# Optimization experiments

Measured on AMD Instinct MI355X. Metric: run time of the kernel, lower is better.

Reference implementation:

```python
import jax, jax.numpy as jnp
from jax import lax
import numpy as np

T, B, I, H, O = 512, 64, 512, 1024, 512


def setup_inputs() -> dict:
    key = jax.random.key(0)
    ks = jax.random.split(key, 8)
    s_ih = 1.0 / np.sqrt(I)
    s_hh = 1.0 / np.sqrt(H)
    return {
        "x": jax.random.normal(ks[0], (T, B, I), dtype=jnp.float32),
        "hidden": jnp.zeros((1, B, H), dtype=jnp.float32),
        "W_ih": jax.random.normal(ks[1], (H, I), dtype=jnp.float32) * s_ih,
        "W_hh": jax.random.normal(ks[2], (H, H), dtype=jnp.float32) * s_hh,
        "b_ih": jax.random.normal(ks[3], (H,), dtype=jnp.float32) * s_hh,
        "b_hh": jax.random.normal(ks[4], (H,), dtype=jnp.float32) * s_hh,
        "W_fc": jax.random.normal(ks[5], (O, H), dtype=jnp.float32) * s_hh,
        "b_fc": jax.random.normal(ks[6], (O,), dtype=jnp.float32) * s_hh,
    }


def reference(x, hidden, W_ih, W_hh, b_ih, b_hh, W_fc, b_fc):
    # Precompute the input projection for all timesteps as one big GEMM.
    # xp: [T, B, H]
    xp = jnp.einsum("tbi,hi->tbh", x, W_ih) + b_ih

    h0 = hidden[0]  # [B, H]

    def step(h, xt):
        # PyTorch RNN (tanh): h_t = tanh(W_ih x_t + b_ih + W_hh h_{t-1} + b_hh)
        h_new = jnp.tanh(xt + h @ W_hh.T + b_hh)
        return h_new, h_new

    h_last, hs = lax.scan(step, h0, xp)  # hs: [T, B, H]

    # fc applied to flattened [T*B, H] hidden states
    out = hs.reshape(-1, hs.shape[-1]) @ W_fc.T + b_fc  # [T*B, O]
    return out, h_last[None]  # ([T*B, O], [1, B, H])
```

## Files before the change

kernel.cpp:

```cpp
#include <hip/hip_runtime.h>

typedef __attribute__((ext_vector_type(8))) short bf16x8;
typedef __attribute__((ext_vector_type(4))) float f32x4;

#define T_N 512
#define I_N 512
#define H_N 1024
#define O_N 512
#define NMEM 16
#define NTHR 512
#define COLS_H 64
#define COLS_FC 32
#define KW 192
#define KWFC 128
#define AP_STRIDE 1544
#define RST 21

__device__ __forceinline__ unsigned short f2bf(float f) {
  unsigned int u = __float_as_uint(f);
  u += 0x7fffu + ((u >> 16) & 1u);
  return (unsigned short)(u >> 16);
}
__device__ __forceinline__ bf16x8 cvt8f(const float* __restrict__ p) {
  float4 a = *(const float4*)p;
  float4 b = *(const float4*)(p + 4);
  bf16x8 r;
  r[0] = (short)f2bf(a.x); r[1] = (short)f2bf(a.y);
  r[2] = (short)f2bf(a.z); r[3] = (short)f2bf(a.w);
  r[4] = (short)f2bf(b.x); r[5] = (short)f2bf(b.y);
  r[6] = (short)f2bf(b.z); r[7] = (short)f2bf(b.w);
  return r;
}

__device__ __forceinline__ void coh_store_b32(unsigned int* p, unsigned int v) {
  asm volatile("global_store_dword %0, %1, off sc0 sc1" :: "v"(p), "v"(v) : "memory");
}
__device__ __forceinline__ unsigned int coh_load_b32(const unsigned int* p) {
  unsigned int r;
  asm volatile("global_load_dword %0, %1, off sc0 sc1\n\t"
               "s_waitcnt vmcnt(0)" : "=v"(r) : "v"(p) : "memory");
  return r;
}

__global__ __launch_bounds__(NTHR, 2) void rnn_fused(
    const float* __restrict__ x, const float* __restrict__ hidden,
    const float* __restrict__ Wih, const float* __restrict__ Whh,
    const float* __restrict__ bih, const float* __restrict__ bhh,
    const float* __restrict__ Wfc, const float* __restrict__ bfc,
    float* __restrict__ out, float* __restrict__ hlast,
    unsigned short* __restrict__ hx, unsigned int* __restrict__ flags)
{
  __shared__ __align__(16) unsigned short Apan[16 * AP_STRIDE];
  __shared__ __align__(16) float R [8 * COLS_H  * RST];
  __shared__ __align__(16) float R2[8 * COLS_FC * RST];

  const int tid = threadIdx.x;
  const int l = tid & 63, w = tid >> 6;
  const int bid = blockIdx.x;
  const int c = bid & 3;
  const int m = bid >> 2;
  const int b0 = c * 16;
  const int cbh = m * COLS_H;
  const int cbfc = m * COLS_FC;
  unsigned short* hxc = hx + (size_t)c * 2 * 16 * H_N;
  unsigned int* flg = flags + c * 64;

  bf16x8 Bh[6][4];
  {
    const int kb0 = w * KW + ((l >> 4) << 3);
#pragma unroll
    for (int kst = 0; kst < 6; ++kst) {
      const int k = kb0 + kst * 32;
#pragma unroll
      for (int f = 0; f < 4; ++f) {
        const int col = cbh + f * 16 + (l & 15);
        const float* src = (k < H_N) ? (Whh + (size_t)col * H_N + k)
                                     : (Wih + (size_t)col * I_N + (k - H_N));
        Bh[kst][f] = cvt8f(src);
      }
    }
  }
  bf16x8 Bf[4][2];
  {
    const int kb0 = w * KWFC + ((l >> 4) << 3);
#pragma unroll
    for (int kst = 0; kst < 4; ++kst)
#pragma unroll
      for (int f = 0; f < 2; ++f) {
        const int col = cbfc + f * 16 + (l & 15);
        Bf[kst][f] = cvt8f(Wfc + (size_t)col * H_N + kb0 + kst * 32);
      }
  }

  const int hrow = (w << 1) + (l >> 5);
  const int hcp  = l & 31;
  const float pb0 = bih[cbh + 2 * hcp]     + bhh[cbh + 2 * hcp];
  const float pb1 = bih[cbh + 2 * hcp + 1] + bhh[cbh + 2 * hcp + 1];
  const int frow = hrow;
  const int fcol = l & 31;
  const float bfv = bfc[cbfc + fcol];

  const int q0 = tid, q1 = 512 + tid;

#pragma unroll
  for (int i = 0; i < 4; ++i) {
    const int q = i * 512 + tid;
    const int row = q >> 7, hc8 = (q & 127) << 3;
    bf16x8 v = cvt8f(hidden + (size_t)(b0 + row) * H_N + hc8);
    *(bf16x8*)(Apan + row * AP_STRIDE + hc8) = v;
  }
  *(bf16x8*)(Apan + (q0 >> 6) * AP_STRIDE + H_N + ((q0 & 63) << 3)) =
      cvt8f(x + (size_t)(b0 + (q0 >> 6)) * I_N + ((q0 & 63) << 3));
  *(bf16x8*)(Apan + (q1 >> 6) * AP_STRIDE + H_N + ((q1 & 63) << 3)) =
      cvt8f(x + (size_t)(b0 + (q1 >> 6)) * I_N + ((q1 & 63) << 3));
  bf16x8 xr0 = cvt8f(x + (size_t)(64 + b0 + (q0 >> 6)) * I_N + ((q0 & 63) << 3));
  bf16x8 xr1 = cvt8f(x + (size_t)(64 + b0 + (q1 >> 6)) * I_N + ((q1 & 63) << 3));
  __syncthreads();

  for (int t = 0; t < T_N; ++t) {
    {
      f32x4 acc[4] = {};
      const int abase = (l & 15) * AP_STRIDE + w * KW + ((l >> 4) << 3);
#pragma unroll
      for (int kst = 0; kst < 6; ++kst) {
        bf16x8 a = *(const bf16x8*)(Apan + abase + kst * 32);
#pragma unroll
        for (int f = 0; f < 4; ++f)
          acc[f] = __builtin_amdgcn_mfma_f32_16x16x32_bf16(a, Bh[kst][f], acc[f], 0, 0, 0);
      }
#pragma unroll
      for (int f = 0; f < 4; ++f)
        *(f32x4*)(R + (size_t)(w * COLS_H + f * 16 + (l & 15)) * RST + ((l >> 4) << 2)) = acc[f];
    }
    if (t > 0) {
      f32x4 afc[2] = {};
      const int ab2 = (l & 15) * AP_STRIDE + w * KWFC + ((l >> 4) << 3);
#pragma unroll
      for (int kst = 0; kst < 4; ++kst) {
        bf16x8 a = *(const bf16x8*)(Apan + ab2 + kst * 32);
        afc[0] = __builtin_amdgcn_mfma_f32_16x16x32_bf16(a, Bf[kst][0], afc[0], 0, 0, 0);
        afc[1] = __builtin_amdgcn_mfma_f32_16x16x32_bf16(a, Bf[kst][1], afc[1], 0, 0, 0);
      }
#pragma unroll
      for (int f = 0; f < 2; ++f)
        *(f32x4*)(R2 + (size_t)(w * COLS_FC + f * 16 + (l & 15)) * RST + ((l >> 4) << 2)) = afc[f];
    }
    __syncthreads();

    {
      float v0 = pb0, v1 = pb1;
#pragma unroll
      for (int kk = 0; kk < 8; ++kk) {
        v0 += R[(size_t)(kk * COLS_H + 2 * hcp)     * RST + hrow];
        v1 += R[(size_t)(kk * COLS_H + 2 * hcp + 1) * RST + hrow];
      }
      const float h0 = tanhf(v0), h1 = tanhf(v1);
      const unsigned int packed =
          (unsigned int)f2bf(h0) | ((unsigned int)f2bf(h1) << 16);
      unsigned int* dst = (unsigned int*)(hxc + (size_t)((t & 1) * 16 + hrow) * H_N + cbh + 2 * hcp);
      coh_store_b32(dst, packed);
      if (t == T_N - 1) {
        float2 fv; fv.x = h0; fv.y = h1;
        *(float2*)(hlast + (size_t)(b0 + hrow) * H_N + cbh + 2 * hcp) = fv;
      }
    }
    asm volatile("s_waitcnt vmcnt(0)" ::: "memory");
    __syncthreads();
    if (tid == 0) coh_store_b32(&flg[m], (unsigned int)(t + 1));

    if (t > 0) {
      float v = bfv;
#pragma unroll
      for (int kk = 0; kk < 8; ++kk)
        v += R2[(size_t)(kk * COLS_FC + fcol) * RST + frow];
      out[(size_t)((t - 1) * 64 + b0 + frow) * O_N + cbfc + fcol] = v;
    }
    if (t + 1 < T_N) {
      *(bf16x8*)(Apan + (q0 >> 6) * AP_STRIDE + H_N + ((q0 & 63) << 3)) = xr0;
      *(bf16x8*)(Apan + (q1 >> 6) * AP_STRIDE + H_N + ((q1 & 63) << 3)) = xr1;
      if (t + 2 < T_N) {
        xr0 = cvt8f(x + (size_t)((t + 2) * 64 + b0 + (q0 >> 6)) * I_N + ((q0 & 63) << 3));
        xr1 = cvt8f(x + (size_t)((t + 2) * 64 + b0 + (q1 >> 6)) * I_N + ((q1 & 63) << 3));
      }
    }

    if (tid < NMEM) {
      while (coh_load_b32(&flg[tid]) < (unsigned int)(t + 1))
        __builtin_amdgcn_s_sleep(1);
    }
    __syncthreads();

    {
      const unsigned long long* src =
          (const unsigned long long*)(hxc + (size_t)(t & 1) * 16 * H_N);
      unsigned long long hv[8];
#pragma unroll
      for (int i = 0; i < 8; ++i)
        asm volatile("global_load_dwordx2 %0, %1, off sc0 sc1"
                     : "=v"(hv[i]) : "v"(src + tid + 512 * i) : "memory");
      asm volatile("s_waitcnt vmcnt(0)" ::: "memory");
      __builtin_amdgcn_sched_barrier(0);
#pragma unroll
      for (int i = 0; i < 8; ++i) {
        const int c8 = tid + 512 * i;
        const int row = c8 >> 8, col = (c8 & 255) << 2;
        *(unsigned long long*)(Apan + row * AP_STRIDE + col) = hv[i];
      }
    }
    __syncthreads();
  }

  {
    f32x4 afc[2] = {};
    const int ab2 = (l & 15) * AP_STRIDE + w * KWFC + ((l >> 4) << 3);
#pragma unroll
    for (int kst = 0; kst < 4; ++kst) {
      bf16x8 a = *(const bf16x8*)(Apan + ab2 + kst * 32);
      afc[0] = __builtin_amdgcn_mfma_f32_16x16x32_bf16(a, Bf[kst][0], afc[0], 0, 0, 0);
      afc[1] = __builtin_amdgcn_mfma_f32_16x16x32_bf16(a, Bf[kst][1], afc[1], 0, 0, 0);
    }
#pragma unroll
    for (int f = 0; f < 2; ++f)
      *(f32x4*)(R2 + (size_t)(w * COLS_FC + f * 16 + (l & 15)) * RST + ((l >> 4) << 2)) = afc[f];
    __syncthreads();
    float v = bfv;
#pragma unroll
    for (int kk = 0; kk < 8; ++kk)
      v += R2[(size_t)(kk * COLS_FC + fcol) * RST + frow];
    out[(size_t)(511 * 64 + b0 + frow) * O_N + cbfc + fcol] = v;
  }
}

extern "C" void kernel_launch(void* const* d_in, const int* in_sizes, int n_in,
                              void* d_out, int out_size, void* d_ws, size_t ws_size,
                              hipStream_t stream) {
  const float* x   = (const float*)d_in[0];
  const float* hid = (const float*)d_in[1];
  const float* Wih = (const float*)d_in[2];
  const float* Whh = (const float*)d_in[3];
  const float* bih = (const float*)d_in[4];
  const float* bhh = (const float*)d_in[5];
  const float* Wfc = (const float*)d_in[6];
  const float* bfc = (const float*)d_in[7];

  float* out   = (float*)d_out;
  float* hlast = out + (size_t)32768 * 512;

  unsigned int*   flags = (unsigned int*)d_ws;
  unsigned short* hx    = (unsigned short*)((char*)d_ws + 1024);

  hipMemsetAsync(flags, 0, 1024, stream);
  rnn_fused<<<64, NTHR, 0, stream>>>(x, hid, Wih, Whh, bih, bhh, Wfc, bfc,
                                     out, hlast, hx, flags);
}
```

Baseline: 1.795 ms.

## Split batch across 8 clusters and replace flag barrier with canary-polled data slots

Doubles the grid to 128 blocks, with each cluster now handling 8 batch rows instead of 16; the MFMA A panel is zero-padded to 16 rows. The per-step flag barrier is replaced by fp32 hidden-state slots in a 4-deep ring. Consumers poll the data itself until no canary values remain, and producers re-poison the slot two steps ahead, which removes a full store-wait, syncthreads and flag round trip per step. Wave specialisation assigns the tanh work to waves 0-3 and the x prefetch to waves 4-7; the costs are wasted MFMA work on padding rows, fp32 traffic instead of bf16, and bounded spin caps that could silently proceed on a timeout.

Result: no change. 1.801 ms (+0.4%).

```diff
diff --git a/kernel.cpp b/kernel.cpp
--- a/kernel.cpp
+++ b/kernel.cpp
@@ -2,19 +2,26 @@
 
 typedef __attribute__((ext_vector_type(8))) short bf16x8;
 typedef __attribute__((ext_vector_type(4))) float f32x4;
+typedef __attribute__((ext_vector_type(2))) float f32x2;
 
 #define T_N 512
 #define I_N 512
 #define H_N 1024
 #define O_N 512
+#define NCL 8
 #define NMEM 16
+#define BATCH 8
 #define NTHR 512
 #define COLS_H 64
 #define COLS_FC 32
 #define KW 192
 #define KWFC 128
 #define AP_STRIDE 1544
-#define RST 21
+#define AP_ROWS 20
+#define RST 9
+#define CANARY 0xFFFFFFFFu
+#define HS_CAP  20000000
+#define POLL_CAP 200000
 
 __device__ __forceinline__ unsigned short f2bf(float f) {
   unsigned int u = __float_as_uint(f);
@@ -31,15 +38,35 @@
   r[6] = (short)f2bf(b.z); r[7] = (short)f2bf(b.w);
   return r;
 }
-
-__device__ __forceinline__ void coh_store_b32(unsigned int* p, unsigned int v) {
+__device__ __forceinline__ bf16x8 cvt8v(float4 a, float4 b) {
+  bf16x8 r;
+  r[0] = (short)f2bf(a.x); r[1] = (short)f2bf(a.y);
+  r[2] = (short)f2bf(a.z); r[3] = (short)f2bf(a.w);
+  r[4] = (short)f2bf(b.x); r[5] = (short)f2bf(b.y);
+  r[6] = (short)f2bf(b.z); r[7] = (short)f2bf(b.w);
+  return r;
+}
+
+__device__ __forceinline__ void st_sc01(unsigned int* p, unsigned int v) {
   asm volatile("global_store_dword %0, %1, off sc0 sc1" :: "v"(p), "v"(v) : "memory");
 }
-__device__ __forceinline__ unsigned int coh_load_b32(const unsigned int* p) {
+__device__ __forceinline__ void st2_sc01(float* p, f32x2 v) {
+  asm volatile("global_store_dwordx2 %0, %1, off sc0 sc1" :: "v"(p), "v"(v) : "memory");
+}
+__device__ __forceinline__ void st2u_sc01(float* p, unsigned long long v) {
+  asm volatile("global_store_dwordx2 %0, %1, off sc0 sc1" :: "v"(p), "v"(v) : "memory");
+}
+__device__ __forceinline__ unsigned int ld_sc01(const unsigned int* p) {
   unsigned int r;
-  asm volatile("global_load_dword %0, %1, off sc0 sc1\n\t"
-               "s_waitcnt vmcnt(0)" : "=v"(r) : "v"(p) : "memory");
+  asm volatile("global_load_dword %0, %1, off sc0 sc1\n\ts_waitcnt vmcnt(0)"
+               : "=v"(r) : "v"(p) : "memory");
   return r;
+}
+__device__ __forceinline__ void ld4_sc01(uint4* d, const void* p) {
+  asm volatile("global_load_dwordx4 %0, %1, off sc0 sc1" : "=v"(*d) : "v"(p) : "memory");
+}
+__device__ __forceinline__ void ld4_rawf(float4* d, const void* p) {
+  asm volatile("global_load_dwordx4 %0, %1, off" : "=v"(*d) : "v"(p) : "memory");
 }
 
 __global__ __launch_bounds__(NTHR, 2) void rnn_fused(
@@ -48,26 +75,25 @@
     const float* __restrict__ bih, const float* __restrict__ bhh,
     const float* __restrict__ Wfc, const float* __restrict__ bfc,
     float* __restrict__ out, float* __restrict__ hlast,
-    unsigned short* __restrict__ hx, unsigned int* __restrict__ flags)
+    float* __restrict__ hslot, unsigned int* __restrict__ flags)
 {
-  __shared__ __align__(16) unsigned short Apan[16 * AP_STRIDE];
+  __shared__ __align__(16) unsigned short Apan[AP_ROWS * AP_STRIDE];
   __shared__ __align__(16) float R [8 * COLS_H  * RST];
   __shared__ __align__(16) float R2[8 * COLS_FC * RST];
 
   const int tid = threadIdx.x;
-  const int l = tid & 63, w = tid >> 6;
+  const int l = tid & 63, wv = tid >> 6;
   const int bid = blockIdx.x;
-  const int c = bid & 3;
-  const int m = bid >> 2;
-  const int b0 = c * 16;
+  const int c = bid & 7;
+  const int m = bid >> 3;
+  const int b0 = c * BATCH;
   const int cbh = m * COLS_H;
   const int cbfc = m * COLS_FC;
-  unsigned short* hxc = hx + (size_t)c * 2 * 16 * H_N;
-  unsigned int* flg = flags + c * 64;
+  float* slotc = hslot + (size_t)c * 4 * BATCH * H_N;
 
   bf16x8 Bh[6][4];
   {
-    const int kb0 = w * KW + ((l >> 4) << 3);
+    const int kb0 = wv * KW + ((l >> 4) << 3);
 #pragma unroll
     for (int kst = 0; kst < 6; ++kst) {
       const int k = kb0 + kst * 32;
@@ -82,45 +108,64 @@
   }
   bf16x8 Bf[4][2];
   {
-    const int kb0 = w * KWFC + ((l >> 4) << 3);
+    const int kb0 = wv * KWFC + ((l >> 4) << 3);
 #pragma unroll
     for (int kst = 0; kst < 4; ++kst)
 #pragma unroll
-      for (int f = 0; f < 2; ++f) {
-        const int col = cbfc + f * 16 + (l & 15);
-        Bf[kst][f] = cvt8f(Wfc + (size_t)col * H_N + kb0 + kst * 32);
-      }
-  }
-
-  const int hrow = (w << 1) + (l >> 5);
-  const int hcp  = l & 31;
-  const float pb0 = bih[cbh + 2 * hcp]     + bhh[cbh + 2 * hcp];
-  const float pb1 = bih[cbh + 2 * hcp + 1] + bhh[cbh + 2 * hcp + 1];
-  const int frow = hrow;
-  const int fcol = l & 31;
-  const float bfv = bfc[cbfc + fcol];
-
-  const int q0 = tid, q1 = 512 + tid;
-
-#pragma unroll
-  for (int i = 0; i < 4; ++i) {
-    const int q = i * 512 + tid;
-    const int row = q >> 7, hc8 = (q & 127) << 3;
-    bf16x8 v = cvt8f(hidden + (size_t)(b0 + row) * H_N + hc8);
-    *(bf16x8*)(Apan + row * AP_STRIDE + hc8) = v;
-  }
-  *(bf16x8*)(Apan + (q0 >> 6) * AP_STRIDE + H_N + ((q0 & 63) << 3)) =
-      cvt8f(x + (size_t)(b0 + (q0 >> 6)) * I_N + ((q0 & 63) << 3));
-  *(bf16x8*)(Apan + (q1 >> 6) * AP_STRIDE + H_N + ((q1 & 63) << 3)) =
-      cvt8f(x + (size_t)(b0 + (q1 >> 6)) * I_N + ((q1 & 63) << 3));
-  bf16x8 xr0 = cvt8f(x + (size_t)(64 + b0 + (q0 >> 6)) * I_N + ((q0 & 63) << 3));
-  bf16x8 xr1 = cvt8f(x + (size_t)(64 + b0 + (q1 >> 6)) * I_N + ((q1 & 63) << 3));
+      for (int f = 0; f < 2; ++f)
+        Bf[kst][f] = cvt8f(Wfc + (size_t)(cbfc + f * 16 + (l & 15)) * H_N + kb0 + kst * 32);
+  }
+
+  const int rrow = (tid >> 5) & 7;
+  const int rcp  = tid & 31;
+  const float pb0 = bih[cbh + 2 * rcp]     + bhh[cbh + 2 * rcp];
+  const float pb1 = bih[cbh + 2 * rcp + 1] + bhh[cbh + 2 * rcp + 1];
+  const float bfv = bfc[cbfc + rcp];
+
+  for (int q = tid; q < (8 * AP_STRIDE) / 4; q += NTHR)
+    ((unsigned long long*)(Apan + 8 * AP_STRIDE))[q] = 0ULL;
+  {
+    int q = tid;
+#pragma unroll
+    for (int i = 0; i < 2; ++i, q += NTHR) {
+      const int row = q >> 7, col8 = (q & 127) << 3;
+      *(bf16x8*)(Apan + row * AP_STRIDE + col8) =
+          cvt8f(hidden + (size_t)(b0 + row) * H_N + col8);
+    }
+  }
+  {
+    const int row = tid >> 6, col8 = (tid & 63) << 3;
+    *(bf16x8*)(Apan + row * AP_STRIDE + H_N + col8) =
+        cvt8f(x + (size_t)(b0 + row) * I_N + col8);
+  }
+  float4 xf0, xf1, xf2, xf3;
+  if (wv >= 4) {
+    const int u = tid & 255;
+    const float* p0 = x + ((size_t)64 + b0 + (u >> 6)) * I_N + ((u & 63) << 3);
+    ld4_rawf(&xf0, p0); ld4_rawf(&xf1, p0 + 4);
+    ld4_rawf(&xf2, p0 + 4 * I_N); ld4_rawf(&xf3, p0 + 4 * I_N + 4);
+  }
+
+  if (tid < 256) {
+#pragma unroll
+    for (int s = 0; s < 4; ++s)
+      st2u_sc01(slotc + (size_t)(s * BATCH + rrow) * H_N + cbh + 2 * rcp,
+                0xFFFFFFFFFFFFFFFFull);
+  }
+  asm volatile("s_waitcnt vmcnt(0)" ::: "memory");
+  __syncthreads();
+  if (tid == 0) st_sc01(&flags[c * 64 + m], 1u);
+  if (tid < NMEM) {
+    int it = 0;
+    while (ld_sc01(&flags[c * 64 + tid]) < 1u && ++it < HS_CAP)
+      if (it > 64) __builtin_amdgcn_s_sleep(1);
+  }
   __syncthreads();
 
   for (int t = 0; t < T_N; ++t) {
     {
       f32x4 acc[4] = {};
-      const int abase = (l & 15) * AP_STRIDE + w * KW + ((l >> 4) << 3);
+      const int abase = (l & 15) * AP_STRIDE + wv * KW + ((l >> 4) << 3);
 #pragma unroll
       for (int kst = 0; kst < 6; ++kst) {
         bf16x8 a = *(const bf16x8*)(Apan + abase + kst * 32);
@@ -128,106 +173,113 @@
         for (int f = 0; f < 4; ++f)
           acc[f] = __builtin_amdgcn_mfma_f32_16x16x32_bf16(a, Bh[kst][f], acc[f], 0, 0, 0);
       }
-#pragma unroll
-      for (int f = 0; f < 4; ++f)
-        *(f32x4*)(R + (size_t)(w * COLS_H + f * 16 + (l & 15)) * RST + ((l >> 4) << 2)) = acc[f];
+      if (l < 32) {
+#pragma unroll
+        for (int f = 0; f < 4; ++f)
+          *(f32x4*)(R + (size_t)(wv * COLS_H + f * 16 + (l & 15)) * RST + ((l >> 4) << 2)) = acc[f];
+      }
     }
     if (t > 0) {
       f32x4 afc[2] = {};
-      const int ab2 = (l & 15) * AP_STRIDE + w * KWFC + ((l >> 4) << 3);
+      const int ab2 = (l & 15) * AP_STRIDE + wv * KWFC + ((l >> 4) << 3);
 #pragma unroll
       for (int kst = 0; kst < 4; ++kst) {
         bf16x8 a = *(const bf16x8*)(Apan + ab2 + kst * 32);
         afc[0] = __builtin_amdgcn_mfma_f32_16x16x32_bf16(a, Bf[kst][0], afc[0], 0, 0, 0);
         afc[1] = __builtin_amdgcn_mfma_f32_16x16x32_bf16(a, Bf[kst][1], afc[1], 0, 0, 0);
       }
-#pragma unroll
-      for (int f = 0; f < 2; ++f)
-        *(f32x4*)(R2 + (size_t)(w * COLS_FC + f * 16 + (l & 15)) * RST + ((l >> 4) << 2)) = afc[f];
+      if (l < 32) {
+        *(f32x4*)(R2 + (size_t)(wv * COLS_FC + (l & 15)) * RST + ((l >> 4) << 2)) = afc[0];
+        *(f32x4*)(R2 + (size_t)(wv * COLS_FC + 16 + (l & 15)) * RST + ((l >> 4) << 2)) = afc[1];
+      }
     }
     __syncthreads();
 
-    {
+    if (wv < 4) {
       float v0 = pb0, v1 = pb1;
 #pragma unroll
       for (int kk = 0; kk < 8; ++kk) {
-        v0 += R[(size_t)(kk * COLS_H + 2 * hcp)     * RST + hrow];
-        v1 += R[(size_t)(kk * COLS_H + 2 * hcp + 1) * RST + hrow];
+        v0 += R[(size_t)(kk * COLS_H + 2 * rcp)     * RST + rrow];
+        v1 += R[(size_t)(kk * COLS_H + 2 * rcp + 1) * RST + rrow];
       }
       const float h0 = tanhf(v0), h1 = tanhf(v1);
-      const unsigned int packed =
-          (unsigned int)f2bf(h0) | ((unsigned int)f2bf(h1) << 16);
-      unsigned int* dst = (unsigned int*)(hxc + (size_t)((t & 1) * 16 + hrow) * H_N + cbh + 2 * hcp);
-      coh_store_b32(dst, packed);
+      f32x2 hv; hv[0] = h0; hv[1] = h1;
+      st2_sc01(slotc + (size_t)((t & 3) * BATCH + rrow) * H_N + cbh + 2 * rcp, hv);
+      st2u_sc01(slotc + (size_t)(((t + 2) & 3) * BATCH + rrow) * H_N + cbh + 2 * rcp,
+                0xFFFFFFFFFFFFFFFFull);
       if (t == T_N - 1) {
         float2 fv; fv.x = h0; fv.y = h1;
-        *(float2*)(hlast + (size_t)(b0 + hrow) * H_N + cbh + 2 * hcp) = fv;
-      }
-    }
-    asm volatile("s_waitcnt vmcnt(0)" ::: "memory");
+        *(float2*)(hlast + (size_t)(b0 + rrow) * H_N + cbh + 2 * rcp) = fv;
+      }
+    } else {
+      if (t + 1 < T_N) {
+        asm volatile("s_waitcnt vmcnt(0)" ::: "memory");
+        const int u = tid & 255;
+        *(bf16x8*)(Apan + (u >> 6) * AP_STRIDE + H_N + ((u & 63) << 3)) = cvt8v(xf0, xf1);
+        *(bf16x8*)(Apan + ((u >> 6) + 4) * AP_STRIDE + H_N + ((u & 63) << 3)) = cvt8v(xf2, xf3);
+        if (t + 2 < T_N) {
+          const float* p0 = x + ((size_t)(t + 2) * 64 + b0 + (u >> 6)) * I_N + ((u & 63) << 3);
+          ld4_rawf(&xf0, p0); ld4_rawf(&xf1, p0 + 4);
+          ld4_rawf(&xf2, p0 + 4 * I_N); ld4_rawf(&xf3, p0 + 4 * I_N + 4);
+        }
+      }
+    }
+
+    if (t > 0 && tid < 256) {
+      float v = bfv;
+#pragma unroll
+      for (int kk = 0; kk < 8; ++kk)
+        v += R2[(size_t)(kk * COLS_FC + rcp) * RST + rrow];
+      out[(size_t)((t - 1) * 64 + b0 + rrow) * O_N + cbfc + rcp] = v;
+    }
+
+    {
+      const float* slotR = slotc + (size_t)(t & 3) * BATCH * H_N;
+      const uint4* sp = (const uint4*)slotR + tid * 4;
+      uint4 u0, u1, u2, u3;
+      int it = 0;
+      while (true) {
+        ld4_sc01(&u0, sp); ld4_sc01(&u1, sp + 1);
+        ld4_sc01(&u2, sp + 2); ld4_sc01(&u3, sp + 3);
+        asm volatile("s_waitcnt vmcnt(0)" ::: "memory");
+        const bool bad =
+            (u0.x == CANARY) | (u0.y == CANARY) | (u0.z == CANARY) | (u0.w == CANARY) |
+            (u1.x == CANARY) | (u1.y == CANARY) | (u1.z == CANARY) | (u1.w == CANARY) |
+            (u2.x == CANARY) | (u2.y == CANARY) | (u2.z == CANARY) | (u2.w == CANARY) |
+            (u3.x == CANARY) | (u3.y == CANARY) | (u3.z == CANARY) | (u3.w == CANARY);
+        if (!bad || ++it >= POLL_CAP) break;
+        __builtin_amdgcn_s_sleep(1);
+      }
+      const int row = tid >> 6, colw = (tid & 63) << 4;
+      float4 f0 = *(float4*)&u0, f1 = *(float4*)&u1;
+      float4 f2 = *(float4*)&u2, f3 = *(float4*)&u3;
+      *(bf16x8*)(Apan + row * AP_STRIDE + colw)     = cvt8v(f0, f1);
+      *(bf16x8*)(Apan + row * AP_STRIDE + colw + 8) = cvt8v(f2, f3);
+    }
     __syncthreads();
-    if (tid == 0) coh_store_b32(&flg[m], (unsigned int)(t + 1));
-
-    if (t > 0) {
-      float v = bfv;
-#pragma unroll
-      for (int kk = 0; kk < 8; ++kk)
-        v += R2[(size_t)(kk * COLS_FC + fcol) * RST + frow];
-      out[(size_t)((t - 1) * 64 + b0 + frow) * O_N + cbfc + fcol] = v;
-    }
-    if (t + 1 < T_N) {
-      *(bf16x8*)(Apan + (q0 >> 6) * AP_STRIDE + H_N + ((q0 & 63) << 3)) = xr0;
-      *(bf16x8*)(Apan + (q1 >> 6) * AP_STRIDE + H_N + ((q1 & 63) << 3)) = xr1;
-      if (t + 2 < T_N) {
-        xr0 = cvt8f(x + (size_t)((t + 2) * 64 + b0 + (q0 >> 6)) * I_N + ((q0 & 63) << 3));
-        xr1 = cvt8f(x + (size_t)((t + 2) * 64 + b0 + (q1 >> 6)) * I_N + ((q1 & 63) << 3));
-      }
-    }
-
-    if (tid < NMEM) {
-      while (coh_load_b32(&flg[tid]) < (unsigned int)(t + 1))
-        __builtin_amdgcn_s_sleep(1);
-    }
-    __syncthreads();
-
-    {
-      const unsigned long long* src =
-          (const unsigned long long*)(hxc + (size_t)(t & 1) * 16 * H_N);
-      unsigned long long hv[8];
-#pragma unroll
-      for (int i = 0; i < 8; ++i)
-        asm volatile("global_load_dwordx2 %0, %1, off sc0 sc1"
-                     : "=v"(hv[i]) : "v"(src + tid + 512 * i) : "memory");
-      asm volatile("s_waitcnt vmcnt(0)" ::: "memory");
-      __builtin_amdgcn_sched_barrier(0);
-#pragma unroll
-      for (int i = 0; i < 8; ++i) {
-        const int c8 = tid + 512 * i;
-        const int row = c8 >> 8, col = (c8 & 255) << 2;
-        *(unsigned long long*)(Apan + row * AP_STRIDE + col) = hv[i];
-      }
-    }
-    __syncthreads();
   }
 
   {
     f32x4 afc[2] = {};
-    const int ab2 = (l & 15) * AP_STRIDE + w * KWFC + ((l >> 4) << 3);
+    const int ab2 = (l & 15) * AP_STRIDE + wv * KWFC + ((l >> 4) << 3);
 #pragma unroll
     for (int kst = 0; kst < 4; ++kst) {
       bf16x8 a = *(const bf16x8*)(Apan + ab2 + kst * 32);
       afc[0] = __builtin_amdgcn_mfma_f32_16x16x32_bf16(a, Bf[kst][0], afc[0], 0, 0, 0);
       afc[1] = __builtin_amdgcn_mfma_f32_16x16x32_bf16(a, Bf[kst][1], afc[1], 0, 0, 0);
     }
-#pragma unroll
-    for (int f = 0; f < 2; ++f)
-      *(f32x4*)(R2 + (size_t)(w * COLS_FC + f * 16 + (l & 15)) * RST + ((l >> 4) << 2)) = afc[f];
+    if (l < 32) {
+      *(f32x4*)(R2 + (size_t)(wv * COLS_FC + (l & 15)) * RST + ((l >> 4) << 2)) = afc[0];
+      *(f32x4*)(R2 + (size_t)(wv * COLS_FC + 16 + (l & 15)) * RST + ((l >> 4) << 2)) = afc[1];
+    }
     __syncthreads();
-    float v = bfv;
-#pragma unroll
-    for (int kk = 0; kk < 8; ++kk)
-      v += R2[(size_t)(kk * COLS_FC + fcol) * RST + frow];
-    out[(size_t)(511 * 64 + b0 + frow) * O_N + cbfc + fcol] = v;
+    if (tid < 256) {
+      float v = bfv;
+#pragma unroll
+      for (int kk = 0; kk < 8; ++kk)
+        v += R2[(size_t)(kk * COLS_FC + rcp) * RST + rrow];
+      out[(size_t)(511 * 64 + b0 + rrow) * O_N + cbfc + rcp] = v;
+    }
   }
 }
 
@@ -246,10 +298,10 @@
   float* out   = (float*)d_out;
   float* hlast = out + (size_t)32768 * 512;
 
-  unsigned int*   flags = (unsigned int*)d_ws;
-  unsigned short* hx    = (unsigned short*)((char*)d_ws + 1024);
-
-  hipMemsetAsync(flags, 0, 1024, stream);
-  rnn_fused<<<64, NTHR, 0, stream>>>(x, hid, Wih, Whh, bih, bhh, Wfc, bfc,
-                                     out, hlast, hx, flags);
-}
+  unsigned int* flags = (unsigned int*)d_ws;
+  float*        hslot = (float*)((char*)d_ws + 4096);
+
+  hipMemsetAsync(flags, 0, 4096, stream);
+  rnn_fused<<<128, NTHR, 0, stream>>>(x, hid, Wih, Whh, bih, bhh, Wfc, bfc,
+                                      out, hlast, hslot, flags);
+}
```
